# Kernel optimization log

Measured on AMD Instinct MI355X. Metric: run time of the kernel, lower is better.

Reference implementation:

```python
import jax, jax.numpy as jnp
import numpy as np

VOCAB, EMBED, HIDDEN, OUT = 32000, 512, 1024, 1
B, T = 256, 512


def setup_inputs() -> dict:
    key = jax.random.key(0)
    ks = jax.random.split(key, 8)
    s_e, s_h = 1.0 / np.sqrt(EMBED), 1.0 / np.sqrt(HIDDEN)
    return {
        "x": jax.random.randint(ks[0], (B, T), 0, VOCAB, dtype=jnp.int64),
        "hidden": jnp.zeros((B, HIDDEN), dtype=jnp.float32),
        "seq_len": jax.random.randint(ks[1], (B,), 1, T + 1, dtype=jnp.int64),
        "embedding": jax.random.normal(ks[2], (VOCAB, EMBED), dtype=jnp.float32),
        "W_ih": jax.random.uniform(ks[3], (3 * HIDDEN, EMBED), jnp.float32, -s_h, s_h),
        "W_hh": jax.random.uniform(ks[4], (3 * HIDDEN, HIDDEN), jnp.float32, -s_h, s_h),
        "b_ih": jax.random.uniform(ks[5], (3 * HIDDEN,), jnp.float32, -s_h, s_h),
        "b_hh": jax.random.uniform(ks[6], (3 * HIDDEN,), jnp.float32, -s_h, s_h),
        "W_lin": jax.random.uniform(ks[7], (OUT, HIDDEN), jnp.float32, -s_h, s_h),
        "b_lin": jnp.zeros((OUT,), dtype=jnp.float32),
    }


def _gru_scan(embeds_tbe, h0, W_ih, W_hh, b_ih, b_hh, W_lin, b_lin):
    # embeds_tbe: [T, B, E]; returns (final hidden [B,H], per-step linear outs [T,B,O])
    def step(h, x_t):
        gi = x_t @ W_ih.T + b_ih            # [B, 3H]
        gh = h @ W_hh.T + b_hh              # [B, 3H]
        i_r, i_z, i_n = jnp.split(gi, 3, axis=-1)
        h_r, h_z, h_n = jnp.split(gh, 3, axis=-1)
        r = jax.nn.sigmoid(i_r + h_r)
        z = jax.nn.sigmoid(i_z + h_z)
        n = jnp.tanh(i_n + r * h_n)
        h_new = (1.0 - z) * n + z * h
        return h_new, h_new @ W_lin.T + b_lin
    return jax.lax.scan(step, h0, embeds_tbe)


def reference(x, hidden, seq_len, embedding, W_ih, W_hh, b_ih, b_hh, W_lin, b_lin):
    batch_size = x.shape[0]
    embeds = embedding[x]                       # [B, T, E]
    h_final, outs = _gru_scan(jnp.swapaxes(embeds, 0, 1), hidden,
                              W_ih, W_hh, b_ih, b_hh, W_lin, b_lin)  # outs: [T, B, O]
    # gather outputs[seq_len[i]-1][i] for each sample
    out = outs[seq_len - 1, jnp.arange(batch_size)]   # [B, O]
    sig_out = jax.nn.sigmoid(out).reshape(batch_size, -1)[:, -1]
    return (sig_out, h_final)
```

## Files before the change

### kernel.cpp

```cpp
#include <hip/hip_runtime.h>

namespace {
constexpr int kB = 256;
constexpr int kT = 512;
constexpr int kE = 512;
constexpr int kH = 1024;
constexpr int BB = 16;
constexpr int NC = 96;
constexpr int CK = 64;
constexpr int NT = 256;
constexpr int F4H = BB * (CK / 4);
constexpr int NPF = (BB + NC) * (CK / 4) / NT;
constexpr int VOCAB = 32000;
}

__global__ void __launch_bounds__(NT, 2)
gru_step(const int* __restrict__ x, const int* __restrict__ seq_len,
         const float* __restrict__ emb, const float* __restrict__ Wih,
         const float* __restrict__ Whh, const float* __restrict__ bih,
         const float* __restrict__ bhh, const float* __restrict__ Wlin,
         const float* __restrict__ blin, const float* __restrict__ hc,
         float* __restrict__ hn, float* __restrict__ out, int t)
{
    __shared__ float h_s[BB][CK + 4];
    __shared__ float w_s[NC][CK + 4];
    __shared__ float gI[NC][BB + 1];
    __shared__ float gH[NC][BB + 1];
    __shared__ float red[NT];
    __shared__ int   sx[BB];
    __shared__ int   ssl[BB];

    const int tid = threadIdx.x;
    const int bg  = blockIdx.x >> 5;
    const int jg  = blockIdx.x & 31;
    const int b0  = bg * BB;
    const int j0  = jg * 32;

    const int tb = (tid & 7) * 2;
    const int tc = (tid >> 3) * 3;
    const int gj = tid & 31;
    const int gb = (tid >> 5) * 2;

    if (tid < BB) {
        ssl[tid] = seq_len[b0 + tid];
        int v = x[(size_t)(b0 + tid) * kT + t];
        sx[tid] = (v >= 0 && v < VOCAB) ? v : 0;
    }
    __syncthreads();

    if (jg == 0 && t > 0) {
        for (int b = 0; b < BB; ++b) {
            if (ssl[b] == t) {
                const float* hr = hc + (size_t)(b0 + b) * kH;
                float p = 0.f;
                for (int k = tid; k < kH; k += NT) p += hr[k] * Wlin[k];
                red[tid] = p;
                __syncthreads();
                for (int s = NT / 2; s > 0; s >>= 1) {
                    if (tid < s) red[tid] += red[tid + s];
                    __syncthreads();
                }
                if (tid == 0) out[b0 + b] = 1.f / (1.f + expf(-(red[0] + blin[0])));
                __syncthreads();
            }
        }
    }

    float bI[3], bH[3];
    #pragma unroll
    for (int j = 0; j < 3; ++j) {
        int c = tc + j;
        int wrow = (c >> 5) * kH + j0 + (c & 31);
        bI[j] = bih[wrow];
        bH[j] = bhh[wrow];
    }

    float4 pf[NPF];

    auto stage_commit = [&]() {
        #pragma unroll
        for (int l = 0; l < NPF; ++l) {
            int idx = l * NT + tid;
            if (idx < F4H) {
                int r = idx >> 4, q = idx & 15;
                *(float4*)&h_s[r][q * 4] = pf[l];
            } else {
                int m = idx - F4H;
                int r = m >> 4, q = m & 15;
                *(float4*)&w_s[r][q * 4] = pf[l];
            }
        }
    };
    auto issue_ih = [&](int k0) {
        #pragma unroll
        for (int l = 0; l < NPF; ++l) {
            int idx = l * NT + tid;
            if (idx < F4H) {
                int r = idx >> 4, q = idx & 15;
                pf[l] = *(const float4*)&emb[(size_t)sx[r] * kE + k0 + q * 4];
            } else {
                int m = idx - F4H;
                int r = m >> 4, q = m & 15;
                int wrow = (r >> 5) * kH + j0 + (r & 31);
                pf[l] = *(const float4*)&Wih[(size_t)wrow * kE + k0 + q * 4];
            }
        }
    };
    auto issue_hh = [&](int k0) {
        #pragma unroll
        for (int l = 0; l < NPF; ++l) {
            int idx = l * NT + tid;
            if (idx < F4H) {
                int r = idx >> 4, q = idx & 15;
                pf[l] = *(const float4*)&hc[(size_t)(b0 + r) * kH + k0 + q * 4];
            } else {
                int m = idx - F4H;
                int r = m >> 4, q = m & 15;
                int wrow = (r >> 5) * kH + j0 + (r & 31);
                pf[l] = *(const float4*)&Whh[(size_t)wrow * kH + k0 + q * 4];
            }
        }
    };
    auto gemm_chunk = [&](float (*acc)[3]) {
        #pragma unroll 2
        for (int kk = 0; kk < CK; kk += 4) {
            float4 hv[2], wv[3];
            #pragma unroll
            for (int i = 0; i < 2; ++i) hv[i] = *(const float4*)&h_s[tb + i][kk];
            #pragma unroll
            for (int j = 0; j < 3; ++j) wv[j] = *(const float4*)&w_s[tc + j][kk];
            #pragma unroll
            for (int i = 0; i < 2; ++i)
                #pragma unroll
                for (int j = 0; j < 3; ++j) {
                    acc[i][j] = fmaf(hv[i].x, wv[j].x, acc[i][j]);
                    acc[i][j] = fmaf(hv[i].y, wv[j].y, acc[i][j]);
                    acc[i][j] = fmaf(hv[i].z, wv[j].z, acc[i][j]);
                    acc[i][j] = fmaf(hv[i].w, wv[j].w, acc[i][j]);
                }
        }
    };

    float ai[2][3], ah[2][3];
    #pragma unroll
    for (int i = 0; i < 2; ++i)
        #pragma unroll
        for (int j = 0; j < 3; ++j) { ai[i][j] = 0.f; ah[i][j] = 0.f; }

    issue_ih(0);
    for (int k0 = 0; k0 < kE; k0 += CK) {
        __syncthreads();
        stage_commit();
        if (k0 + CK < kE) issue_ih(k0 + CK);
        __syncthreads();
        gemm_chunk(ai);
    }

    issue_hh(0);
    for (int k0 = 0; k0 < kH; k0 += CK) {
        __syncthreads();
        stage_commit();
        if (k0 + CK < kH) issue_hh(k0 + CK);
        __syncthreads();
        gemm_chunk(ah);
    }

    __syncthreads();
    #pragma unroll
    for (int j = 0; j < 3; ++j) {
        int c = tc + j;
        #pragma unroll
        for (int i = 0; i < 2; ++i) {
            gI[c][tb + i] = ai[i][j] + bI[j];
            gH[c][tb + i] = ah[i][j] + bH[j];
        }
    }
    __syncthreads();

    #pragma unroll
    for (int i = 0; i < 2; ++i) {
        int b = gb + i;
        float xr = gI[gj][b] + gH[gj][b];
        float xz = gI[32 + gj][b] + gH[32 + gj][b];
        float rr = 1.f / (1.f + expf(-xr));
        float zz = 1.f / (1.f + expf(-xz));
        float nn = tanhf(gI[64 + gj][b] + rr * gH[64 + gj][b]);
        size_t off = (size_t)(b0 + b) * kH + j0 + gj;
        float hold = hc[off];
        hn[off] = (1.f - zz) * nn + zz * hold;
    }
}

__global__ void __launch_bounds__(NT)
gru_final(const float* __restrict__ hf, const int* __restrict__ seq_len,
          const float* __restrict__ Wlin, const float* __restrict__ blin,
          float* __restrict__ out)
{
    __shared__ float red[NT];
    const int b = blockIdx.x, tid = threadIdx.x;
    const float* hr = hf + (size_t)b * kH;

    float4 v = *(const float4*)&hr[tid * 4];
    *(float4*)&out[kB + (size_t)b * kH + tid * 4] = v;

    if (seq_len[b] == kT) {
        float4 w = *(const float4*)&Wlin[tid * 4];
        red[tid] = v.x * w.x + v.y * w.y + v.z * w.z + v.w * w.w;
        __syncthreads();
        for (int s = NT / 2; s > 0; s >>= 1) {
            if (tid < s) red[tid] += red[tid + s];
            __syncthreads();
        }
        if (tid == 0) out[b] = 1.f / (1.f + expf(-(red[0] + blin[0])));
    }
}

extern "C" void kernel_launch(void* const* d_in, const int* in_sizes, int n_in,
                              void* d_out, int out_size, void* d_ws, size_t ws_size,
                              hipStream_t stream) {
    (void)in_sizes; (void)n_in; (void)out_size; (void)ws_size;
    const int*   x    = (const int*)  d_in[0];
    const float* h0   = (const float*)d_in[1];
    const int*   sl   = (const int*)  d_in[2];
    const float* emb  = (const float*)d_in[3];
    const float* Wih  = (const float*)d_in[4];
    const float* Whh  = (const float*)d_in[5];
    const float* bih  = (const float*)d_in[6];
    const float* bhh  = (const float*)d_in[7];
    const float* Wlin = (const float*)d_in[8];
    const float* blin = (const float*)d_in[9];
    float* out  = (float*)d_out;
    float* buf0 = (float*)d_ws;
    float* buf1 = (float*)d_ws + (size_t)kB * kH;

    for (int t = 0; t < kT; ++t) {
        const float* hc = (t == 0) ? h0 : ((t & 1) ? buf1 : buf0);
        float* hn = ((t + 1) & 1) ? buf1 : buf0;
        hipLaunchKernelGGL(gru_step, dim3(512), dim3(NT), 0, stream,
                           x, sl, emb, Wih, Whh, bih, bhh, Wlin, blin,
                           hc, hn, out, t);
    }
    hipLaunchKernelGGL(gru_final, dim3(kB), dim3(NT), 0, stream,
                       buf0, sl, Wlin, blin, out);
}
```

Baseline: 58.32 ms.

## Use split-bf16x3 MFMA for GRU step GEMMs with prepacked weights

Replaces the fp32 FMA GEMM in each GRU timestep with bf16 MFMA instructions, representing each fp32 operand as a sum of three bf16 values and accumulating six cross products to keep near-fp32 accuracy. Weights and biases are prepacked once per call into an MFMA-friendly layout. Each step also writes its new hidden state, plus the next timestep's embedding, in pre-split bf16 form for the following step. This targets the scalar FMA throughput bound, at the cost of extra prep kernels, more bandwidth from triple-plane operands, and fewer blocks per step. The new path runs only when the workspace is large enough; otherwise the old kernel is used.

```diff
diff --git a/kernel.cpp b/kernel.cpp
--- a/kernel.cpp
+++ b/kernel.cpp
@@ -1,45 +1,394 @@
 #include <hip/hip_runtime.h>
+#include <hip/hip_bf16.h>
+
+typedef __attribute__((ext_vector_type(8))) short short8;
+typedef __attribute__((ext_vector_type(4))) float f32x4;
 
 namespace {
-constexpr int kB = 256;
-constexpr int kT = 512;
-constexpr int kE = 512;
-constexpr int kH = 1024;
-constexpr int BB = 16;
-constexpr int NC = 96;
-constexpr int CK = 64;
+constexpr int kB = 256, kT = 512, kE = 512, kH = 1024;
+constexpr int CH = 48;
 constexpr int NT = 256;
+constexpr int VOCAB = 32000;
+
+constexpr size_t W_ELEMS = (size_t)32 * CH * 12 * 96 * 8;
+constexpr size_t X_ELEMS_BUF = (size_t)CH * 12 * 256 * 8;
+constexpr size_t OFF_W = 0;
+constexpr size_t OFF_X = W_ELEMS * 2;
+constexpr size_t OFF_H = OFF_X + X_ELEMS_BUF * 2 * 2;
+constexpr size_t OFF_BIAS = OFF_H + (size_t)2 * kB * kH * 4;
+constexpr size_t WS_NEED = OFF_BIAS + (size_t)32 * 2 * 96 * 4;
+}
+
+__device__ __forceinline__ unsigned short f2bf(float f) {
+    __hip_bfloat16 h = __float2bfloat16(f);
+    return *reinterpret_cast<unsigned short*>(&h);
+}
+__device__ __forceinline__ float bf2f(unsigned short u) {
+    __hip_bfloat16 h = *reinterpret_cast<__hip_bfloat16*>(&u);
+    return __bfloat162float(h);
+}
+
+#define MFMA16(A_, B_, C_) __builtin_amdgcn_mfma_f32_16x16x32_bf16((A_), (B_), (C_), 0, 0, 0)
+
+__global__ void __launch_bounds__(256)
+prep_w(const float* __restrict__ Wih, const float* __restrict__ Whh,
+       const float* __restrict__ bih, const float* __restrict__ bhh,
+       unsigned short* __restrict__ wsW, float* __restrict__ wsBias)
+{
+    const int blk = blockIdx.x;
+    const int jg = blk / CH, c = blk % CH;
+    const int tid = threadIdx.x;
+
+    for (int u0 = tid; u0 < 384; u0 += 256) {
+        int col = u0 >> 2, kg = u0 & 3;
+        int type = (col % 48) >> 4;
+        int uu = (col / 48) * 16 + (col & 15);
+        int grow = type * kH + jg * 32 + uu;
+        float v[8];
+        if (c < 32) {
+            int kb = c * 32 + kg * 8;
+            const float4* p = (const float4*)&Whh[(size_t)grow * kH + kb];
+            float4 x0 = p[0], x1 = p[1];
+            v[0]=x0.x; v[1]=x0.y; v[2]=x0.z; v[3]=x0.w;
+            v[4]=x1.x; v[5]=x1.y; v[6]=x1.z; v[7]=x1.w;
+        } else {
+            int kb = (c - 32) * 32 + kg * 8;
+            const float4* p = (const float4*)&Wih[(size_t)grow * kE + kb];
+            float4 x0 = p[0], x1 = p[1];
+            v[0]=x0.x; v[1]=x0.y; v[2]=x0.z; v[3]=x0.w;
+            v[4]=x1.x; v[5]=x1.y; v[6]=x1.z; v[7]=x1.w;
+        }
+        size_t base = ((size_t)blk * 12 + kg) * 768 + (size_t)col * 8;
+        #pragma unroll
+        for (int e = 0; e < 8; ++e) {
+            float xx = v[e];
+            unsigned short q0 = f2bf(xx);
+            float r1 = xx - bf2f(q0);
+            unsigned short q1 = f2bf(r1);
+            unsigned short q2 = f2bf(r1 - bf2f(q1));
+            wsW[base + e]            = q0;
+            wsW[base + 4 * 768 + e]  = q1;
+            wsW[base + 8 * 768 + e]  = q2;
+        }
+    }
+    if (c == 0 && tid < 96) {
+        int col = tid;
+        int type = (col % 48) >> 4;
+        int uu = (col / 48) * 16 + (col & 15);
+        int grow = type * kH + jg * 32 + uu;
+        wsBias[(jg * 2 + 0) * 96 + col] = bih[grow];
+        wsBias[(jg * 2 + 1) * 96 + col] = bhh[grow];
+    }
+}
+
+__global__ void __launch_bounds__(256)
+prep_x0(const int* __restrict__ x, const float* __restrict__ h0,
+        const float* __restrict__ emb, unsigned short* __restrict__ wsX,
+        float* __restrict__ wsH)
+{
+    const int c = blockIdx.x;
+    const int tid = threadIdx.x;
+    #pragma unroll 2
+    for (int l = 0; l < 12; ++l) {
+        int unit = l * 256 + tid;
+        int plkg = unit >> 8, b = unit & 255;
+        int pl = plkg >> 2, kg = plkg & 3;
+        float v[8];
+        if (c < 32) {
+            int j = c * 32 + kg * 8;
+            const float4* p = (const float4*)&h0[(size_t)b * kH + j];
+            float4 x0 = p[0], x1 = p[1];
+            v[0]=x0.x; v[1]=x0.y; v[2]=x0.z; v[3]=x0.w;
+            v[4]=x1.x; v[5]=x1.y; v[6]=x1.z; v[7]=x1.w;
+            if (pl == 0) {
+                #pragma unroll
+                for (int e = 0; e < 8; ++e) wsH[(size_t)b * kH + j + e] = v[e];
+            }
+        } else {
+            int tok = x[(size_t)b * kT];
+            tok = (tok >= 0 && tok < VOCAB) ? tok : 0;
+            int ke = (c - 32) * 32 + kg * 8;
+            const float4* p = (const float4*)&emb[(size_t)tok * kE + ke];
+            float4 x0 = p[0], x1 = p[1];
+            v[0]=x0.x; v[1]=x0.y; v[2]=x0.z; v[3]=x0.w;
+            v[4]=x1.x; v[5]=x1.y; v[6]=x1.z; v[7]=x1.w;
+        }
+        size_t base = ((size_t)c * 12 + plkg) * 2048 + (size_t)b * 8;
+        #pragma unroll
+        for (int e = 0; e < 8; ++e) {
+            float xx = v[e];
+            unsigned short q0 = f2bf(xx);
+            float r1 = xx - bf2f(q0);
+            unsigned short q1 = f2bf(r1);
+            unsigned short q2 = f2bf(r1 - bf2f(q1));
+            unsigned short q = (pl == 0) ? q0 : ((pl == 1) ? q1 : q2);
+            wsX[base + e] = q;
+        }
+    }
+}
+
+__global__ void __launch_bounds__(NT, 1)
+gru_step_mfma(const int* __restrict__ x, const int* __restrict__ seq_len,
+              const float* __restrict__ emb, const float* __restrict__ Wlin,
+              const float* __restrict__ blin,
+              const unsigned short* __restrict__ wsW,
+              const float* __restrict__ wsBias,
+              unsigned short* __restrict__ wsX, float* __restrict__ wsH,
+              float* __restrict__ out, int t)
+{
+    __shared__ __align__(16) short lds[49152];
+    __shared__ float red[NT];
+    __shared__ int ssl[32];
+
+    const int tid = threadIdx.x;
+    const int bg = blockIdx.x >> 5, jg = blockIdx.x & 31;
+    const int b0 = bg * 32;
+    const int w = tid >> 6, lane = tid & 63, lid = lane & 15, kg = lane >> 4;
+
+    const int bufR = t & 1, bufW = bufR ^ 1;
+    const unsigned short* Xr = wsX + (size_t)bufR * X_ELEMS_BUF;
+    unsigned short* Xw = wsX + (size_t)bufW * X_ELEMS_BUF;
+    const float* Hr = wsH + (size_t)bufR * kB * kH;
+    float* Hw = wsH + (size_t)bufW * kB * kH;
+
+    if (tid < 32) ssl[tid] = seq_len[b0 + tid];
+    __syncthreads();
+
+    if (jg == 0 && t > 0) {
+        for (int b = 0; b < 32; ++b) {
+            if (ssl[b] == t) {
+                const float* hr = Hr + (size_t)(b0 + b) * kH;
+                float p = 0.f;
+                for (int k = tid; k < kH; k += NT) p += hr[k] * Wlin[k];
+                red[tid] = p;
+                __syncthreads();
+                for (int s = NT / 2; s > 0; s >>= 1) {
+                    if (tid < s) red[tid] += red[tid + s];
+                    __syncthreads();
+                }
+                if (tid == 0) out[b0 + b] = 1.f / (1.f + expf(-(red[0] + blin[0])));
+                __syncthreads();
+            }
+        }
+    }
+
+    const int4* gW = (const int4*)wsW;
+    const int4* gX = (const int4*)Xr;
+    int4* lA = (int4*)lds;
+    int4* lB = (int4*)(lds + 12288);
+    int4 pf[12];
+
+    auto issue = [&](int pair) {
+        #pragma unroll
+        for (int l = 0; l < 12; ++l) {
+            int u = l * 256 + tid;
+            int hi = (u >= 1536);
+            int cc = 2 * pair + hi;
+            int v = u - (hi ? 1536 : 0);
+            if (v < 1152) {
+                pf[l] = gW[(size_t)(jg * CH + cc) * 1152 + v];
+            } else {
+                int wv = v - 1152;
+                pf[l] = gX[(size_t)(cc * 12 + (wv >> 5)) * 256 + (b0 + (wv & 31))];
+            }
+        }
+    };
+    auto commit = [&](int pair) {
+        #pragma unroll
+        for (int l = 0; l < 12; ++l) {
+            int u = l * 256 + tid;
+            int hi = (u >= 1536);
+            int cc = 2 * pair + hi;
+            int v = u - (hi ? 1536 : 0);
+            if (v < 1152) lB[(cc & 3) * 1152 + v] = pf[l];
+            else          lA[(cc & 3) * 384 + (v - 1152)] = pf[l];
+        }
+    };
+
+    f32x4 zz4 = {0.f, 0.f, 0.f, 0.f};
+    f32x4 ar[2] = {zz4, zz4}, az[2] = {zz4, zz4};
+    f32x4 anh[2] = {zz4, zz4}, ani[2] = {zz4, zz4};
+    const int pr = w >> 1, half = w & 1;
+
+    auto compute = [&](int c) {
+        const short* A = lds + (c & 3) * 3072;
+        const short* B = lds + 12288 + (c & 3) * 9216;
+        short8 fa[3][2], fb[3][3];
+        #pragma unroll
+        for (int pl = 0; pl < 3; ++pl) {
+            #pragma unroll
+            for (int rg = 0; rg < 2; ++rg)
+                fa[pl][rg] = *(const short8*)&A[(pl * 4 + kg) * 256 + (rg * 16 + lid) * 8];
+            #pragma unroll
+            for (int cg = 0; cg < 3; ++cg)
+                fb[pl][cg] = *(const short8*)&B[(pl * 4 + kg) * 768 + (half * 48 + cg * 16 + lid) * 8];
+        }
+        const int TA[6] = {0, 0, 1, 0, 2, 1};
+        const int TB[6] = {0, 1, 0, 2, 0, 1};
+        #pragma unroll
+        for (int s = 0; s < 6; ++s) {
+            #pragma unroll
+            for (int rg = 0; rg < 2; ++rg) {
+                ar[rg] = MFMA16(fa[TA[s]][rg], fb[TB[s]][0], ar[rg]);
+                az[rg] = MFMA16(fa[TA[s]][rg], fb[TB[s]][1], az[rg]);
+            }
+        }
+        if (c < 32) {
+            #pragma unroll
+            for (int s = 0; s < 6; ++s)
+                #pragma unroll
+                for (int rg = 0; rg < 2; ++rg)
+                    anh[rg] = MFMA16(fa[TA[s]][rg], fb[TB[s]][2], anh[rg]);
+        } else {
+            #pragma unroll
+            for (int s = 0; s < 6; ++s)
+                #pragma unroll
+                for (int rg = 0; rg < 2; ++rg)
+                    ani[rg] = MFMA16(fa[TA[s]][rg], fb[TB[s]][2], ani[rg]);
+        }
+    };
+
+    issue(0);
+    commit(0);
+    __syncthreads();
+    issue(1);
+    for (int i = 0; i < 24; ++i) {
+        compute(2 * i + pr);
+        if (i + 1 < 24) {
+            commit(i + 1);
+            if (i + 2 < 24) issue(i + 2);
+            __syncthreads();
+        }
+    }
+    __syncthreads();
+
+    float* xch = (float*)lds;
+    if (w >= 2) {
+        int base = ((w - 2) * 64 + lane) * 32;
+        #pragma unroll
+        for (int q = 0; q < 4; ++q) {
+            xch[base + 0 + q]  = ar[0][q];  xch[base + 4 + q]  = ar[1][q];
+            xch[base + 8 + q]  = az[0][q];  xch[base + 12 + q] = az[1][q];
+            xch[base + 16 + q] = anh[0][q]; xch[base + 20 + q] = anh[1][q];
+            xch[base + 24 + q] = ani[0][q]; xch[base + 28 + q] = ani[1][q];
+        }
+    }
+    __syncthreads();
+
+    if (w < 2) {
+        int base = (w * 64 + lane) * 32;
+        #pragma unroll
+        for (int q = 0; q < 4; ++q) {
+            ar[0][q]  += xch[base + 0 + q];  ar[1][q]  += xch[base + 4 + q];
+            az[0][q]  += xch[base + 8 + q];  az[1][q]  += xch[base + 12 + q];
+            anh[0][q] += xch[base + 16 + q]; anh[1][q] += xch[base + 20 + q];
+            ani[0][q] += xch[base + 24 + q]; ani[1][q] += xch[base + 28 + q];
+        }
+        const int u = w * 16 + lid;
+        const int j = jg * 32 + u;
+        const float bIr = wsBias[(jg * 2 + 0) * 96 + w * 48 + lid];
+        const float bHr = wsBias[(jg * 2 + 1) * 96 + w * 48 + lid];
+        const float bIz = wsBias[(jg * 2 + 0) * 96 + w * 48 + 16 + lid];
+        const float bHz = wsBias[(jg * 2 + 1) * 96 + w * 48 + 16 + lid];
+        const float bIn = wsBias[(jg * 2 + 0) * 96 + w * 48 + 32 + lid];
+        const float bHn = wsBias[(jg * 2 + 1) * 96 + w * 48 + 32 + lid];
+        size_t xb0 = ((size_t)jg * 12 + (u >> 3)) * 2048 + (u & 7);
+        #pragma unroll
+        for (int rg = 0; rg < 2; ++rg) {
+            #pragma unroll
+            for (int q = 0; q < 4; ++q) {
+                int brow = b0 + rg * 16 + kg * 4 + q;
+                float xr = ar[rg][q] + bIr + bHr;
+                float xz = az[rg][q] + bIz + bHz;
+                float rr = 1.f / (1.f + expf(-xr));
+                float zg = 1.f / (1.f + expf(-xz));
+                float nn = tanhf((ani[rg][q] + bIn) + rr * (anh[rg][q] + bHn));
+                float hold = Hr[(size_t)brow * kH + j];
+                float hv = (1.f - zg) * nn + zg * hold;
+                Hw[(size_t)brow * kH + j] = hv;
+                unsigned short q0 = f2bf(hv);
+                float r1 = hv - bf2f(q0);
+                unsigned short q1 = f2bf(r1);
+                unsigned short q2 = f2bf(r1 - bf2f(q1));
+                size_t xb = xb0 + (size_t)brow * 8;
+                Xw[xb] = q0; Xw[xb + 4 * 2048] = q1; Xw[xb + 8 * 2048] = q2;
+                if (t == kT - 1) out[kB + (size_t)brow * kH + j] = hv;
+            }
+        }
+    } else if (t + 1 < kT) {
+        int ce = jg >> 1, par = jg & 1;
+        int ttt = (w - 2) * 64 + lane;
+        int rrow = ttt >> 3, kg2 = (ttt >> 1) & 3, h4 = ttt & 1;
+        int brow = b0 + par * 16 + rrow;
+        int tok = x[(size_t)brow * kT + (t + 1)];
+        tok = (tok >= 0 && tok < VOCAB) ? tok : 0;
+        int ke = ce * 32 + kg2 * 8 + h4 * 4;
+        float4 v = *(const float4*)&emb[(size_t)tok * kE + ke];
+        float vv[4] = {v.x, v.y, v.z, v.w};
+        size_t base = ((size_t)(32 + ce) * 12 + kg2) * 2048 + (size_t)brow * 8 + h4 * 4;
+        #pragma unroll
+        for (int e = 0; e < 4; ++e) {
+            float xx = vv[e];
+            unsigned short q0 = f2bf(xx);
+            float r1 = xx - bf2f(q0);
+            unsigned short q1 = f2bf(r1);
+            unsigned short q2 = f2bf(r1 - bf2f(q1));
+            Xw[base + e] = q0;
+            Xw[base + 4 * 2048 + e] = q1;
+            Xw[base + 8 * 2048 + e] = q2;
+        }
+    }
+}
+
+__global__ void __launch_bounds__(NT)
+gru_final2(const float* __restrict__ hf, const int* __restrict__ seq_len,
+           const float* __restrict__ Wlin, const float* __restrict__ blin,
+           float* __restrict__ out)
+{
+    __shared__ float red[NT];
+    const int b = blockIdx.x, tid = threadIdx.x;
+    if (seq_len[b] == kT) {
+        const float* hr = hf + (size_t)b * kH;
+        float4 v = *(const float4*)&hr[tid * 4];
+        float4 wv = *(const float4*)&Wlin[tid * 4];
+        red[tid] = v.x * wv.x + v.y * wv.y + v.z * wv.z + v.w * wv.w;
+        __syncthreads();
+        for (int s = NT / 2; s > 0; s >>= 1) {
+            if (tid < s) red[tid] += red[tid + s];
+            __syncthreads();
+        }
+        if (tid == 0) out[b] = 1.f / (1.f + expf(-(red[0] + blin[0])));
+    }
+}
+
+namespace fb {
+constexpr int BB = 16, NC = 96, CK = 64;
 constexpr int F4H = BB * (CK / 4);
 constexpr int NPF = (BB + NC) * (CK / 4) / NT;
-constexpr int VOCAB = 32000;
 }
 
 __global__ void __launch_bounds__(NT, 2)
-gru_step(const int* __restrict__ x, const int* __restrict__ seq_len,
-         const float* __restrict__ emb, const float* __restrict__ Wih,
-         const float* __restrict__ Whh, const float* __restrict__ bih,
-         const float* __restrict__ bhh, const float* __restrict__ Wlin,
-         const float* __restrict__ blin, const float* __restrict__ hc,
-         float* __restrict__ hn, float* __restrict__ out, int t)
+gru_step_fb(const int* __restrict__ x, const int* __restrict__ seq_len,
+            const float* __restrict__ emb, const float* __restrict__ Wih,
+            const float* __restrict__ Whh, const float* __restrict__ bih,
+            const float* __restrict__ bhh, const float* __restrict__ Wlin,
+            const float* __restrict__ blin, const float* __restrict__ hc,
+            float* __restrict__ hn, float* __restrict__ out, int t)
 {
+    using namespace fb;
     __shared__ float h_s[BB][CK + 4];
     __shared__ float w_s[NC][CK + 4];
     __shared__ float gI[NC][BB + 1];
     __shared__ float gH[NC][BB + 1];
     __shared__ float red[NT];
-    __shared__ int   sx[BB];
-    __shared__ int   ssl[BB];
+    __shared__ int sx[BB];
+    __shared__ int ssl[BB];
 
     const int tid = threadIdx.x;
-    const int bg  = blockIdx.x >> 5;
-    const int jg  = blockIdx.x & 31;
-    const int b0  = bg * BB;
-    const int j0  = jg * 32;
-
-    const int tb = (tid & 7) * 2;
-    const int tc = (tid >> 3) * 3;
-    const int gj = tid & 31;
-    const int gb = (tid >> 5) * 2;
+    const int bg = blockIdx.x >> 5, jg = blockIdx.x & 31;
+    const int b0 = bg * BB, j0 = jg * 32;
+    const int tb = (tid & 7) * 2, tc = (tid >> 3) * 3;
+    const int gj = tid & 31, gb = (tid >> 5) * 2;
 
     if (tid < BB) {
         ssl[tid] = seq_len[b0 + tid];
@@ -71,54 +420,38 @@
     for (int j = 0; j < 3; ++j) {
         int c = tc + j;
         int wrow = (c >> 5) * kH + j0 + (c & 31);
-        bI[j] = bih[wrow];
-        bH[j] = bhh[wrow];
+        bI[j] = bih[wrow]; bH[j] = bhh[wrow];
     }
 
     float4 pf[NPF];
-
     auto stage_commit = [&]() {
         #pragma unroll
         for (int l = 0; l < NPF; ++l) {
             int idx = l * NT + tid;
-            if (idx < F4H) {
-                int r = idx >> 4, q = idx & 15;
-                *(float4*)&h_s[r][q * 4] = pf[l];
-            } else {
-                int m = idx - F4H;
-                int r = m >> 4, q = m & 15;
-                *(float4*)&w_s[r][q * 4] = pf[l];
-            }
+            if (idx < F4H) { int r = idx >> 4, q = idx & 15; *(float4*)&h_s[r][q * 4] = pf[l]; }
+            else { int m = idx - F4H; int r = m >> 4, q = m & 15; *(float4*)&w_s[r][q * 4] = pf[l]; }
         }
     };
     auto issue_ih = [&](int k0) {
         #pragma unroll
         for (int l = 0; l < NPF; ++l) {
             int idx = l * NT + tid;
-            if (idx < F4H) {
-                int r = idx >> 4, q = idx & 15;
-                pf[l] = *(const float4*)&emb[(size_t)sx[r] * kE + k0 + q * 4];
-            } else {
-                int m = idx - F4H;
-                int r = m >> 4, q = m & 15;
+            if (idx < F4H) { int r = idx >> 4, q = idx & 15;
+                pf[l] = *(const float4*)&emb[(size_t)sx[r] * kE + k0 + q * 4]; }
+            else { int m = idx - F4H; int r = m >> 4, q = m & 15;
                 int wrow = (r >> 5) * kH + j0 + (r & 31);
-                pf[l] = *(const float4*)&Wih[(size_t)wrow * kE + k0 + q * 4];
-            }
+                pf[l] = *(const float4*)&Wih[(size_t)wrow * kE + k0 + q * 4]; }
         }
     };
     auto issue_hh = [&](int k0) {
         #pragma unroll
         for (int l = 0; l < NPF; ++l) {
             int idx = l * NT + tid;
-            if (idx < F4H) {
-                int r = idx >> 4, q = idx & 15;
-                pf[l] = *(const float4*)&hc[(size_t)(b0 + r) * kH + k0 + q * 4];
-            } else {
-                int m = idx - F4H;
-                int r = m >> 4, q = m & 15;
+            if (idx < F4H) { int r = idx >> 4, q = idx & 15;
+                pf[l] = *(const float4*)&hc[(size_t)(b0 + r) * kH + k0 + q * 4]; }
+            else { int m = idx - F4H; int r = m >> 4, q = m & 15;
                 int wrow = (r >> 5) * kH + j0 + (r & 31);
-                pf[l] = *(const float4*)&Whh[(size_t)wrow * kH + k0 + q * 4];
-            }
+                pf[l] = *(const float4*)&Whh[(size_t)wrow * kH + k0 + q * 4]; }
         }
     };
     auto gemm_chunk = [&](float (*acc)[3]) {
@@ -155,7 +488,6 @@
         __syncthreads();
         gemm_chunk(ai);
     }
-
     issue_hh(0);
     for (int k0 = 0; k0 < kH; k0 += CK) {
         __syncthreads();
@@ -183,29 +515,27 @@
         float xr = gI[gj][b] + gH[gj][b];
         float xz = gI[32 + gj][b] + gH[32 + gj][b];
         float rr = 1.f / (1.f + expf(-xr));
-        float zz = 1.f / (1.f + expf(-xz));
+        float zg = 1.f / (1.f + expf(-xz));
         float nn = tanhf(gI[64 + gj][b] + rr * gH[64 + gj][b]);
         size_t off = (size_t)(b0 + b) * kH + j0 + gj;
         float hold = hc[off];
-        hn[off] = (1.f - zz) * nn + zz * hold;
+        hn[off] = (1.f - zg) * nn + zg * hold;
     }
 }
 
 __global__ void __launch_bounds__(NT)
-gru_final(const float* __restrict__ hf, const int* __restrict__ seq_len,
-          const float* __restrict__ Wlin, const float* __restrict__ blin,
-          float* __restrict__ out)
+gru_final_fb(const float* __restrict__ hf, const int* __restrict__ seq_len,
+             const float* __restrict__ Wlin, const float* __restrict__ blin,
+             float* __restrict__ out)
 {
     __shared__ float red[NT];
     const int b = blockIdx.x, tid = threadIdx.x;
     const float* hr = hf + (size_t)b * kH;
-
     float4 v = *(const float4*)&hr[tid * 4];
     *(float4*)&out[kB + (size_t)b * kH + tid * 4] = v;
-
     if (seq_len[b] == kT) {
-        float4 w = *(const float4*)&Wlin[tid * 4];
-        red[tid] = v.x * w.x + v.y * w.y + v.z * w.z + v.w * w.w;
+        float4 wv = *(const float4*)&Wlin[tid * 4];
+        red[tid] = v.x * wv.x + v.y * wv.y + v.z * wv.z + v.w * wv.w;
         __syncthreads();
         for (int s = NT / 2; s > 0; s >>= 1) {
             if (tid < s) red[tid] += red[tid + s];
@@ -218,7 +548,7 @@
 extern "C" void kernel_launch(void* const* d_in, const int* in_sizes, int n_in,
                               void* d_out, int out_size, void* d_ws, size_t ws_size,
                               hipStream_t stream) {
-    (void)in_sizes; (void)n_in; (void)out_size; (void)ws_size;
+    (void)in_sizes; (void)n_in; (void)out_size;
     const int*   x    = (const int*)  d_in[0];
     const float* h0   = (const float*)d_in[1];
     const int*   sl   = (const int*)  d_in[2];
@@ -229,17 +559,29 @@
     const float* bhh  = (const float*)d_in[7];
     const float* Wlin = (const float*)d_in[8];
     const float* blin = (const float*)d_in[9];
-    float* out  = (float*)d_out;
-    float* buf0 = (float*)d_ws;
-    float* buf1 = (float*)d_ws + (size_t)kB * kH;
-
-    for (int t = 0; t < kT; ++t) {
-        const float* hc = (t == 0) ? h0 : ((t & 1) ? buf1 : buf0);
-        float* hn = ((t + 1) & 1) ? buf1 : buf0;
-        hipLaunchKernelGGL(gru_step, dim3(512), dim3(NT), 0, stream,
-                           x, sl, emb, Wih, Whh, bih, bhh, Wlin, blin,
-                           hc, hn, out, t);
-    }
-    hipLaunchKernelGGL(gru_final, dim3(kB), dim3(NT), 0, stream,
-                       buf0, sl, Wlin, blin, out);
-}
+    float* out = (float*)d_out;
+
+    if (ws_size >= WS_NEED) {
+        unsigned short* wsW = (unsigned short*)((char*)d_ws + OFF_W);
+        unsigned short* wsX = (unsigned short*)((char*)d_ws + OFF_X);
+        float* wsH  = (float*)((char*)d_ws + OFF_H);
+        float* wsBias = (float*)((char*)d_ws + OFF_BIAS);
+
+        prep_w<<<32 * CH, 256, 0, stream>>>(Wih, Whh, bih, bhh, wsW, wsBias);
+        prep_x0<<<CH, 256, 0, stream>>>(x, h0, emb, wsX, wsH);
+        for (int t = 0; t < kT; ++t)
+            gru_step_mfma<<<256, NT, 0, stream>>>(x, sl, emb, Wlin, blin,
+                                                  wsW, wsBias, wsX, wsH, out, t);
+        gru_final2<<<kB, NT, 0, stream>>>(wsH, sl, Wlin, blin, out);
+    } else {
+        float* buf0 = (float*)d_ws;
+        float* buf1 = (float*)d_ws + (size_t)kB * kH;
+        for (int t = 0; t < kT; ++t) {
+            const float* hc = (t == 0) ? h0 : ((t & 1) ? buf1 : buf0);
+            float* hn = ((t + 1) & 1) ? buf1 : buf0;
+            gru_step_fb<<<512, NT, 0, stream>>>(x, sl, emb, Wih, Whh, bih, bhh,
+                                                Wlin, blin, hc, hn, out, t);
+        }
+        gru_final_fb<<<kB, NT, 0, stream>>>(buf0, sl, Wlin, blin, out);
+    }
+}
```

New measurement: 61.22 ms. 5.0% more time.
